# Performance work log

Hardware: AMD Instinct MI355X
Metric: run time of the kernel (lower is better)

The kernel has to match this reference:

```python
import jax, jax.numpy as jnp
import numpy as np

B, S, E, H = 4, 2048, 1024, 16
D = E // H  # head_dim = 64


def setup_inputs() -> dict:
    key = jax.random.key(0)
    k1, k2, k3 = jax.random.split(key, 3)
    x = jax.random.normal(k1, (B, S, E), dtype=jnp.float32)
    w_attn = jax.random.normal(k2, (E, 3 * E), dtype=jnp.float32) * (E ** -0.5)
    b_attn = jnp.zeros((3 * E,), dtype=jnp.float32)
    w_out = jax.random.normal(k3, (E, E), dtype=jnp.float32) * (E ** -0.5)
    b_out = jnp.zeros((E,), dtype=jnp.float32)
    return {"x": x, "w_attn": w_attn, "b_attn": b_attn, "w_out": w_out, "b_out": b_out}


def reference(x, w_attn, b_attn, w_out, b_out):
    b, s, e = x.shape
    qkv = x @ w_attn + b_attn                      # [b, s, 3e]
    q, k, v = jnp.split(qkv, 3, axis=2)
    q = q.reshape(b, s, H, D)
    k = k.reshape(b, s, H, D)
    v = v.reshape(b, s, H, D)
    energy = jnp.einsum('nqhd,nkhd->nhqk', q, k)   # [b, H, s, s]
    causal = jnp.tril(jnp.ones((s, s), dtype=bool))
    energy = jnp.where(causal, energy, -jnp.inf)
    scale = jnp.sqrt(jnp.float32(D))
    attn = jax.nn.softmax(energy / scale, axis=-1)  # dropout_rate=0.0 -> identity
    out = jnp.einsum('nhql,nlhd->nqhd', attn, v).reshape(b, s, e)
    return out @ w_out + b_out
```

## Files before the change

kernel.cpp:

```cpp
#include <hip/hip_runtime.h>

typedef short bf16x8 __attribute__((ext_vector_type(8)));
typedef float f32x4 __attribute__((ext_vector_type(4)));
typedef float f32x16 __attribute__((ext_vector_type(16)));
typedef float float4v __attribute__((ext_vector_type(4)));
typedef short short4v __attribute__((ext_vector_type(4)));
typedef unsigned uint2v __attribute__((ext_vector_type(2)));
typedef unsigned uint4v __attribute__((ext_vector_type(4)));

#define B_ 4
#define S_ 2048
#define E_ 1024
#define H_ 16
#define D_ 64
#define M_ (B_*S_)
#define N1_ (3*E_)

__device__ inline short f2bs(float f) {
    unsigned u = __builtin_bit_cast(unsigned, f);
    unsigned r = u + 0x7fffu + ((u >> 16) & 1u);
    return (short)(r >> 16);
}
__device__ inline float exp2a(float x) {
    float r; asm("v_exp_f32 %0, %1" : "=v"(r) : "v"(x)); return r;
}
__device__ inline unsigned cvtpk(float a, float b) {
    unsigned r; asm("v_cvt_pk_bf16_f32 %0, %1, %2" : "=v"(r) : "v"(a), "v"(b)); return r;
}

__device__ inline const __attribute__((address_space(1))) void* gas(const void* p) {
    return (const __attribute__((address_space(1))) void*)p;
}
__device__ inline __attribute__((address_space(3))) void* las(void* p) {
    return (__attribute__((address_space(3))) void*)p;
}

__global__ void convert_f32_bf16(const float* __restrict__ in, short* __restrict__ out, int n) {
    int tid = blockIdx.x * blockDim.x + threadIdx.x;
    int stride = gridDim.x * blockDim.x;
    for (int i = tid * 4; i < n; i += stride * 4) {
        float4v v = *(const float4v*)&in[i];
        short4v o;
        o[0] = f2bs(v[0]); o[1] = f2bs(v[1]); o[2] = f2bs(v[2]); o[3] = f2bs(v[3]);
        *(short4v*)&out[i] = o;
    }
}

__global__ void transpose_convert(const float* __restrict__ in, short* __restrict__ out,
                                  int rows, int cols) {
    __shared__ float t[32][33];
    int bx = blockIdx.x * 32;
    int by = blockIdx.y * 32;
    int tx = threadIdx.x, ty = threadIdx.y;
#pragma unroll
    for (int i = 0; i < 4; ++i)
        t[ty + i * 8][tx] = in[(size_t)(by + ty + i * 8) * cols + bx + tx];
    __syncthreads();
#pragma unroll
    for (int i = 0; i < 4; ++i)
        out[(size_t)(bx + ty + i * 8) * rows + by + tx] = f2bs(t[tx][ty + i * 8]);
}

#define MFMA12(Q) \
    _Pragma("unroll") for (int mf = 0; mf < 2; ++mf) \
    _Pragma("unroll") for (int nf = 0; nf < 3; ++nf) { \
        acc[(Q)*2+mf][nf] = __builtin_amdgcn_mfma_f32_16x16x32_bf16(af[mf][0], bfrag[nf][0], acc[(Q)*2+mf][nf], 0, 0, 0); \
        acc[(Q)*2+mf][nf] = __builtin_amdgcn_mfma_f32_16x16x32_bf16(af[mf][1], bfrag[nf][1], acc[(Q)*2+mf][nf], 0, 0, 0); \
    }

#define PHASE(Q, STAGE_STMT, WAITV) do { \
    bf16x8 af[2][2]; \
    _Pragma("unroll") for (int mf = 0; mf < 2; ++mf) \
    _Pragma("unroll") for (int ks = 0; ks < 2; ++ks) { \
        int r = (Q)*32 + mf*16 + li; \
        af[mf][ks] = *(const bf16x8*)(lA + r*128 + ((ks*64 + g*16) ^ ((r & 7) << 4))); \
    } \
    STAGE_STMT; \
    __builtin_amdgcn_s_barrier(); \
    asm volatile("s_waitcnt lgkmcnt(0)" ::: "memory"); \
    __builtin_amdgcn_sched_barrier(0); \
    __builtin_amdgcn_s_setprio(1); \
    MFMA12(Q); \
    __builtin_amdgcn_s_setprio(0); \
    WAITV; \
    __builtin_amdgcn_s_barrier(); \
} while (0)

#define VMW(n) asm volatile("s_waitcnt vmcnt(" #n ")" ::: "memory")
#define NOP_ ((void)0)

__global__ __launch_bounds__(512, 2) void gemm_qkv(
    const short* __restrict__ A, const short* __restrict__ Bt,
    const float* __restrict__ bias,
    short* __restrict__ Qb, short* __restrict__ Kb, short* __restrict__ Vt) {
    __shared__ __attribute__((aligned(16))) short ldsA[2][16384];
    __shared__ __attribute__((aligned(16))) short ldsB[2][12288];
    const int tid = threadIdx.x;
    const int lane = tid & 63;
    const int wid = tid >> 6;
    const int li = lane & 15, g = lane >> 4;
    const int wr = wid >> 2, wc = wid & 3;
    const int Kdim = E_;
    const int NT = Kdim >> 6;

    const int id = blockIdx.x;
    const int swz = (id & 7) * 64 + (id >> 3);
    const int bx = swz & 15, by = swz >> 4;
    const int row0 = by * 256, col0 = bx * 192;

    const int rstage = wid * 8 + (lane >> 3);
    const int cstage = (((lane & 7) ^ ((lane >> 3) & 7)) << 4);

    auto stageA = [&](int buf, int kt, int seg) {
#pragma unroll
        for (int h = 0; h < 2; ++h) {
            const char* src = (const char*)A +
                ((size_t)(row0 + h * 128 + seg * 64 + rstage) * Kdim + kt * 64) * 2 + cstage;
            char* dst = (char*)&ldsA[buf][0] + (h * 2 + seg) * 8192 + wid * 1024;
            __builtin_amdgcn_global_load_lds(gas(src), las(dst), 16, 0, 0);
        }
    };
    auto stageB = [&](int buf, int kt) {
#pragma unroll
        for (int i = 0; i < 3; ++i) {
            const char* src = (const char*)Bt +
                ((size_t)(col0 + i * 64 + rstage) * Kdim + kt * 64) * 2 + cstage;
            char* dst = (char*)&ldsB[buf][0] + i * 8192 + wid * 1024;
            __builtin_amdgcn_global_load_lds(gas(src), las(dst), 16, 0, 0);
        }
    };

    f32x4 acc[8][3];
#pragma unroll
    for (int m = 0; m < 8; ++m)
#pragma unroll
        for (int n = 0; n < 3; ++n) acc[m][n] = (f32x4){0.f, 0.f, 0.f, 0.f};

    stageB(0, 0);
    stageA(0, 0, 0);
    stageA(0, 0, 1);
    asm volatile("s_waitcnt vmcnt(0)" ::: "memory");
    __syncthreads();

    for (int t = 0; t < NT; ++t) {
        const int cur = t & 1;
        const int nb = cur ^ 1;
        const int tn = t + 1;
        const bool st = (tn < NT);
        const char* lA = (const char*)&ldsA[cur][0] + wr * 16384;
        const char* lB = (const char*)&ldsB[cur][0];

        bf16x8 bfrag[3][2];
#pragma unroll
        for (int nf = 0; nf < 3; ++nf)
#pragma unroll
            for (int ks = 0; ks < 2; ++ks) {
                int r = wc * 48 + nf * 16 + li;
                bfrag[nf][ks] = *(const bf16x8*)(lB + r * 128 + ((ks * 64 + g * 16) ^ ((r & 7) << 4)));
            }
        if (st) {
            PHASE(0, { stageB(nb, tn); stageA(nb, tn, 0); stageA(nb, tn, 1); }, NOP_);
            PHASE(1, NOP_, VMW(7));
            PHASE(2, NOP_, NOP_);
            PHASE(3, NOP_, VMW(2));
        } else {
            PHASE(0, NOP_, NOP_);
            PHASE(1, NOP_, VMW(0));
            PHASE(2, NOP_, NOP_);
            PHASE(3, NOP_, NOP_);
        }
    }

#pragma unroll
    for (int nf = 0; nf < 3; ++nf) {
        int ncolg = col0 + wc * 48 + nf * 16 + li;
        float bv = bias[ncolg];
        int part = ncolg >> 10;
        int rem = ncolg & 1023;
        if (part < 2) {
            short* Dst = (part == 0) ? Qb : Kb;
#pragma unroll
            for (int mi = 0; mi < 8; ++mi) {
                int rbase = row0 + wr * 128 + mi * 16 + 4 * g;
#pragma unroll
                for (int j = 0; j < 4; ++j)
                    Dst[(size_t)(rbase + j) * E_ + rem] = f2bs(acc[mi][nf][j] + bv);
            }
        } else {
            int h = rem >> 6, d = rem & 63;
#pragma unroll
            for (int mi = 0; mi < 8; ++mi) {
                int s0 = row0 + wr * 128 + mi * 16 + 4 * g;
                int bb2 = s0 >> 11;
                int ss = s0 & 2047;
                uint2v p;
                p[0] = cvtpk(acc[mi][nf][0] + bv, acc[mi][nf][1] + bv);
                p[1] = cvtpk(acc[mi][nf][2] + bv, acc[mi][nf][3] + bv);
                *(uint2v*)&Vt[((size_t)(bb2 * H_ + h) * D_ + d) * S_ + ss] = p;
            }
        }
    }
}

#define MFMA8(Q) \
    _Pragma("unroll") for (int mf = 0; mf < 2; ++mf) \
    _Pragma("unroll") for (int nf = 0; nf < 2; ++nf) { \
        acc[(Q)*2+mf][nf] = __builtin_amdgcn_mfma_f32_16x16x32_bf16(af[mf][0], bfrag[nf][0], acc[(Q)*2+mf][nf], 0, 0, 0); \
        acc[(Q)*2+mf][nf] = __builtin_amdgcn_mfma_f32_16x16x32_bf16(af[mf][1], bfrag[nf][1], acc[(Q)*2+mf][nf], 0, 0, 0); \
    }

#define PHASE8(Q, STAGE_STMT, WAITV) do { \
    bf16x8 af[2][2]; \
    _Pragma("unroll") for (int mf = 0; mf < 2; ++mf) \
    _Pragma("unroll") for (int ks = 0; ks < 2; ++ks) { \
        int r = (Q)*32 + mf*16 + li; \
        af[mf][ks] = *(const bf16x8*)(lA + r*128 + ((ks*64 + g*16) ^ ((r & 7) << 4))); \
    } \
    STAGE_STMT; \
    __builtin_amdgcn_s_barrier(); \
    asm volatile("s_waitcnt lgkmcnt(0)" ::: "memory"); \
    __builtin_amdgcn_sched_barrier(0); \
    __builtin_amdgcn_s_setprio(1); \
    MFMA8(Q); \
    __builtin_amdgcn_s_setprio(0); \
    WAITV; \
    __builtin_amdgcn_s_barrier(); \
} while (0)

__global__ __launch_bounds__(512, 2) void gemm_out8(
    const short* __restrict__ A, const short* __restrict__ Bt,
    const float* __restrict__ bias, float* __restrict__ Cf) {
    __shared__ __attribute__((aligned(16))) short ldsA[2][2][2][4096];
    __shared__ __attribute__((aligned(16))) short ldsB[2][8192];
    const int tid = threadIdx.x;
    const int lane = tid & 63;
    const int wid = tid >> 6;
    const int li = lane & 15, g = lane >> 4;
    const int wr = wid >> 2, wc = wid & 3;
    const int Kdim = E_;
    const int NT = Kdim >> 6;

    const int id = blockIdx.x;
    const int swz = (id & 7) * 32 + (id >> 3);
    const int bx = swz & 7, by = swz >> 3;
    const int row0 = by * 256, col0 = bx * 128;

    const int rstage = wid * 8 + (lane >> 3);
    const int cstage = (((lane & 7) ^ ((lane >> 3) & 7)) << 4);

    auto stageA = [&](int buf, int kt, int seg) {
#pragma unroll
        for (int h = 0; h < 2; ++h) {
            const char* src = (const char*)A +
                ((size_t)(row0 + h * 128 + seg * 64 + rstage) * Kdim + kt * 64) * 2 + cstage;
            char* dst = (char*)&ldsA[buf][h][seg][0] + wid * 1024;
            __builtin_amdgcn_global_load_lds(gas(src), las(dst), 16, 0, 0);
        }
    };
    auto stageB = [&](int buf, int kt) {
#pragma unroll
        for (int i = 0; i < 2; ++i) {
            const char* src = (const char*)Bt +
                ((size_t)(col0 + i * 64 + rstage) * Kdim + kt * 64) * 2 + cstage;
            char* dst = (char*)&ldsB[buf][0] + i * 8192 + wid * 1024;
            __builtin_amdgcn_global_load_lds(gas(src), las(dst), 16, 0, 0);
        }
    };

    f32x4 acc[8][2];
#pragma unroll
    for (int m = 0; m < 8; ++m)
#pragma unroll
        for (int n = 0; n < 2; ++n) acc[m][n] = (f32x4){0.f, 0.f, 0.f, 0.f};

    stageB(0, 0);
    stageA(0, 0, 0);
    stageA(0, 0, 1);
    asm volatile("s_waitcnt vmcnt(0)" ::: "memory");
    __syncthreads();

    for (int t = 0; t < NT; ++t) {
        const int cur = t & 1;
        const int nb = cur ^ 1;
        const int tn = t + 1;
        const bool st = (tn < NT);
        const char* lA = (const char*)&ldsA[cur][wr][0][0];
        const char* lB = (const char*)&ldsB[cur][0];

        bf16x8 bfrag[2][2];
#pragma unroll
        for (int nf = 0; nf < 2; ++nf)
#pragma unroll
            for (int ks = 0; ks < 2; ++ks) {
                int r = wc * 32 + nf * 16 + li;
                bfrag[nf][ks] = *(const bf16x8*)(lB + r * 128 + ((ks * 64 + g * 16) ^ ((r & 7) << 4)));
            }
        if (st) {
            PHASE8(0, stageB(nb, tn), NOP_);
            PHASE8(1, stageA(nb, tn, 0), VMW(4));
            PHASE8(2, stageA(nb, tn, 1), NOP_);
            PHASE8(3, NOP_, VMW(2));
        } else {
            PHASE8(0, NOP_, NOP_);
            PHASE8(1, NOP_, VMW(0));
            PHASE8(2, NOP_, NOP_);
            PHASE8(3, NOP_, NOP_);
        }
    }

#pragma unroll
    for (int nf = 0; nf < 2; ++nf) {
        int ncol = col0 + wc * 32 + nf * 16 + li;
        float bv = bias[ncol];
#pragma unroll
        for (int mi = 0; mi < 8; ++mi) {
            int rbase = row0 + wr * 128 + mi * 16 + 4 * g;
#pragma unroll
            for (int j = 0; j < 4; ++j)
                Cf[(size_t)(rbase + j) * E_ + ncol] = acc[mi][nf][j] + bv;
        }
    }
}

__global__ __launch_bounds__(256, 4) void attn_kernel(
    const short* __restrict__ Qb, const short* __restrict__ Kb,
    const short* __restrict__ Vt, short* __restrict__ Ob) {
    __shared__ __attribute__((aligned(16))) short Kl[4096];
    __shared__ __attribute__((aligned(16))) short Vl[4096];
    const int lane = threadIdx.x & 63;
    const int wv = threadIdx.x >> 6;
    const int l31 = lane & 31;
    const int hi = lane >> 5;
    const int id = blockIdx.x;
    const int xcd = id & 7;
    const int r_ = id >> 3;
    const int qt = 15 - (r_ >> 3);
    const int bh = xcd * 8 + (r_ & 7);
    const int bb = bh >> 4, hh = bh & 15;
    const short* Qh = Qb + (size_t)bb * (S_ * E_) + hh * 64;
    const short* Kh = Kb + (size_t)bb * (S_ * E_) + hh * 64;
    const short* Vh = Vt + (size_t)bh * (D_ * S_);
    const float CEXP = 0.18033688011112042f;

    const int rstage = wv * 8 + (lane >> 3);
    const int cstage = (((lane & 7) ^ ((lane >> 3) & 7)) << 4);

    const int q0w = qt * 128 + wv * 32;
    const int q = q0w + l31;

    bf16x8 qf[4];
#pragma unroll
    for (int c = 0; c < 4; ++c)
        qf[c] = *(const bf16x8*)&Qh[(size_t)q * E_ + c * 16 + hi * 8];

    f32x16 acc[2];
#pragma unroll
    for (int d = 0; d < 2; ++d)
#pragma unroll
        for (int r = 0; r < 16; ++r) acc[d][r] = 0.f;
    float m = -3e38f, mC = 0.f, l = 0.f;

    const int nw = (q0w + 95) >> 6;
    const int nt = (qt * 128 + 191) >> 6;

    for (int it = 0; it < nt; ++it) {
        const int kt0 = it * 64;
#pragma unroll
        for (int half = 0; half < 2; ++half) {
            const char* gk = (const char*)(Kh + (size_t)(kt0 + half * 32 + rstage) * E_) + cstage;
            __builtin_amdgcn_global_load_lds(gas(gk), las((char*)Kl + half * 4096 + wv * 1024), 16, 0, 0);
            const char* gv = (const char*)Vh + (size_t)(half * 32 + rstage) * (S_ * 2) + (size_t)kt0 * 2 + cstage;
            __builtin_amdgcn_global_load_lds(gas(gv), las((char*)Vl + half * 4096 + wv * 1024), 16, 0, 0);
        }
        __syncthreads();
        if (it < nw) {
            f32x16 sc0, sc1;
#pragma unroll
            for (int r = 0; r < 16; ++r) { sc0[r] = 0.f; sc1[r] = 0.f; }
#pragma unroll
            for (int c = 0; c < 4; ++c) {
                const int r0 = l31, r1 = 32 + l31;
                bf16x8 kf0 = *(const bf16x8*)((const char*)Kl + r0 * 128 +
                                              ((c * 32 + hi * 16) ^ ((r0 & 7) << 4)));
                bf16x8 kf1 = *(const bf16x8*)((const char*)Kl + r1 * 128 +
                                              ((c * 32 + hi * 16) ^ ((r1 & 7) << 4)));
                sc0 = __builtin_amdgcn_mfma_f32_32x32x16_bf16(kf0, qf[c], sc0, 0, 0, 0);
                sc1 = __builtin_amdgcn_mfma_f32_32x32x16_bf16(kf1, qf[c], sc1, 0, 0, 0);
            }
            if (kt0 + 63 > q0w) {
                const int kb = kt0 + 4 * hi;
#pragma unroll
                for (int r = 0; r < 16; ++r) {
                    int key = kb + (r & 3) + 8 * (r >> 2);
                    sc0[r] = (key > q) ? -3e38f : sc0[r];
                    sc1[r] = (key + 32 > q) ? -3e38f : sc1[r];
                }
            }
            float tmx[8];
#pragma unroll
            for (int r = 0; r < 8; ++r)
                tmx[r] = fmaxf(fmaxf(sc0[2 * r], sc0[2 * r + 1]),
                               fmaxf(sc1[2 * r], sc1[2 * r + 1]));
            float tm = fmaxf(fmaxf(fmaxf(tmx[0], tmx[1]), fmaxf(tmx[2], tmx[3])),
                             fmaxf(fmaxf(tmx[4], tmx[5]), fmaxf(tmx[6], tmx[7])));
            tm = fmaxf(tm, __shfl_xor(tm, 32, 64));
            bool need = (tm > m + 16.0f);
            if (__ballot((int)need) != 0ull) {
                float mn = fmaxf(m, tm);
                float sf = exp2a((m - mn) * CEXP);
                m = mn; mC = mn * CEXP;
                l *= sf;
#pragma unroll
                for (int d = 0; d < 2; ++d)
#pragma unroll
                    for (int r = 0; r < 16; ++r) acc[d][r] *= sf;
            }
#pragma unroll
            for (int r = 0; r < 16; ++r) {
                sc0[r] = exp2a(fmaf(sc0[r], CEXP, -mC));
                sc1[r] = exp2a(fmaf(sc1[r], CEXP, -mC));
            }
            float s0 = 0.f, s1 = 0.f;
#pragma unroll
            for (int r = 0; r < 8; ++r) {
                s0 += sc0[2 * r] + sc0[2 * r + 1];
                s1 += sc1[2 * r] + sc1[2 * r + 1];
            }
            float ls = s0 + s1;
            ls += __shfl_xor(ls, 32, 64);
            l += ls;
            const bool lo = (hi == 0);
            bf16x8 pf[4];
#pragma unroll
            for (int s = 0; s < 2; ++s) {
                const f32x16& p = s ? sc1 : sc0;
                unsigned W0 = cvtpk(p[0], p[1]),   W1 = cvtpk(p[2], p[3]);
                unsigned W2 = cvtpk(p[4], p[5]),   W3 = cvtpk(p[6], p[7]);
                unsigned W4 = cvtpk(p[8], p[9]),   W5 = cvtpk(p[10], p[11]);
                unsigned W6 = cvtpk(p[12], p[13]), W7 = cvtpk(p[14], p[15]);
                unsigned xW0 = __shfl_xor(W0, 32, 64), xW1 = __shfl_xor(W1, 32, 64);
                unsigned xW2 = __shfl_xor(W2, 32, 64), xW3 = __shfl_xor(W3, 32, 64);
                unsigned xW4 = __shfl_xor(W4, 32, 64), xW5 = __shfl_xor(W5, 32, 64);
                unsigned xW6 = __shfl_xor(W6, 32, 64), xW7 = __shfl_xor(W7, 32, 64);
                uint4v u1, u2;
                u1[0] = lo ? W0 : xW2;  u1[1] = lo ? W1 : xW3;
                u1[2] = lo ? xW0 : W2;  u1[3] = lo ? xW1 : W3;
                u2[0] = lo ? W4 : xW6;  u2[1] = lo ? W5 : xW7;
                u2[2] = lo ? xW4 : W6;  u2[3] = lo ? xW5 : W7;
                pf[s * 2] = __builtin_bit_cast(bf16x8, u1);
                pf[s * 2 + 1] = __builtin_bit_cast(bf16x8, u2);
            }
#pragma unroll
            for (int db = 0; db < 2; ++db) {
                const int row = db * 32 + l31;
                const int rsw = (row & 7) << 4;
                const char* vrow = (const char*)Vl + row * 128;
                bf16x8 v0 = *(const bf16x8*)(vrow + ((hi * 16) ^ rsw));
                bf16x8 v1 = *(const bf16x8*)(vrow + ((32 + hi * 16) ^ rsw));
                bf16x8 v2 = *(const bf16x8*)(vrow + ((64 + hi * 16) ^ rsw));
                bf16x8 v3 = *(const bf16x8*)(vrow + ((96 + hi * 16) ^ rsw));
                acc[db] = __builtin_amdgcn_mfma_f32_32x32x16_bf16(v0, pf[0], acc[db], 0, 0, 0);
                acc[db] = __builtin_amdgcn_mfma_f32_32x32x16_bf16(v1, pf[1], acc[db], 0, 0, 0);
                acc[db] = __builtin_amdgcn_mfma_f32_32x32x16_bf16(v2, pf[2], acc[db], 0, 0, 0);
                acc[db] = __builtin_amdgcn_mfma_f32_32x32x16_bf16(v3, pf[3], acc[db], 0, 0, 0);
            }
        }
        __syncthreads();
    }

    float rl = __builtin_amdgcn_rcpf(l);
    short* orow = Ob + ((size_t)(bb * S_ + q)) * E_ + hh * 64;
#pragma unroll
    for (int db = 0; db < 2; ++db)
#pragma unroll
        for (int rb = 0; rb < 4; ++rb) {
            uint2v pk;
            pk[0] = cvtpk(acc[db][rb * 4 + 0] * rl, acc[db][rb * 4 + 1] * rl);
            pk[1] = cvtpk(acc[db][rb * 4 + 2] * rl, acc[db][rb * 4 + 3] * rl);
            *(uint2v*)&orow[db * 32 + rb * 8 + hi * 4] = pk;
        }
}

extern "C" void kernel_launch(void* const* d_in, const int* in_sizes, int n_in,
                              void* d_out, int out_size, void* d_ws, size_t ws_size,
                              hipStream_t stream) {
    const float* x      = (const float*)d_in[0];
    const float* w_attn = (const float*)d_in[1];
    const float* b_attn = (const float*)d_in[2];
    const float* w_out  = (const float*)d_in[3];
    const float* b_out  = (const float*)d_in[4];
    float* out = (float*)d_out;

    char* ws = (char*)d_ws;
    short* Xbf  = (short*)(ws);
    short* Wat  = (short*)(ws + (16ull << 20));
    short* Wot  = (short*)(ws + (22ull << 20));
    short* Qb   = (short*)(ws + (24ull << 20));
    short* Kb   = (short*)(ws + (40ull << 20));
    short* Vt   = (short*)(ws + (56ull << 20));
    short* Obuf = Xbf;

    convert_f32_bf16<<<2048, 256, 0, stream>>>(x, Xbf, M_ * E_);
    transpose_convert<<<dim3(N1_ / 32, E_ / 32), dim3(32, 8), 0, stream>>>(w_attn, Wat, E_, N1_);
    transpose_convert<<<dim3(E_ / 32, E_ / 32), dim3(32, 8), 0, stream>>>(w_out, Wot, E_, E_);

    gemm_qkv<<<512, 512, 0, stream>>>(Xbf, Wat, b_attn, Qb, Kb, Vt);

    attn_kernel<<<1024, 256, 0, stream>>>(Qb, Kb, Vt, Obuf);

    gemm_out8<<<256, 512, 0, stream>>>(Obuf, Wot, b_out, out);
}
```

Measured before the change: 175.6 us.

## Retile QKV GEMM to 128x192 blocks with 4 waves and 1024 workgroups

```diff
diff --git a/kernel.cpp b/kernel.cpp
--- a/kernel.cpp
+++ b/kernel.cpp
@@ -61,84 +61,82 @@
         out[(size_t)(bx + ty + i * 8) * rows + by + tx] = f2bs(t[tx][ty + i * 8]);
 }
 
-#define MFMA12(Q) \
-    _Pragma("unroll") for (int mf = 0; mf < 2; ++mf) \
-    _Pragma("unroll") for (int nf = 0; nf < 3; ++nf) { \
-        acc[(Q)*2+mf][nf] = __builtin_amdgcn_mfma_f32_16x16x32_bf16(af[mf][0], bfrag[nf][0], acc[(Q)*2+mf][nf], 0, 0, 0); \
-        acc[(Q)*2+mf][nf] = __builtin_amdgcn_mfma_f32_16x16x32_bf16(af[mf][1], bfrag[nf][1], acc[(Q)*2+mf][nf], 0, 0, 0); \
-    }
-
-#define PHASE(Q, STAGE_STMT, WAITV) do { \
-    bf16x8 af[2][2]; \
-    _Pragma("unroll") for (int mf = 0; mf < 2; ++mf) \
-    _Pragma("unroll") for (int ks = 0; ks < 2; ++ks) { \
-        int r = (Q)*32 + mf*16 + li; \
-        af[mf][ks] = *(const bf16x8*)(lA + r*128 + ((ks*64 + g*16) ^ ((r & 7) << 4))); \
-    } \
+#define VMW(n) asm volatile("s_waitcnt vmcnt(" #n ")" ::: "memory")
+#define NOP_ ((void)0)
+
+#define QKV_MFMA(Q) \
+    _Pragma("unroll") for (int nf = 0; nf < 6; ++nf) { \
+        acc[(Q)][nf] = __builtin_amdgcn_mfma_f32_16x16x32_bf16(af[0], bfrag[nf][0], acc[(Q)][nf], 0, 0, 0); \
+        acc[(Q)][nf] = __builtin_amdgcn_mfma_f32_16x16x32_bf16(af[1], bfrag[nf][1], acc[(Q)][nf], 0, 0, 0); \
+    }
+
+#define QKV_PHASE(Q, STAGE_STMT, WAITV) do { \
+    bf16x8 af[2]; \
+    const char* lAq = lA + (Q) * 4096; \
+    _Pragma("unroll") for (int ks = 0; ks < 2; ++ks) \
+        af[ks] = *(const bf16x8*)(lAq + li * 128 + ((ks * 64 + g * 16) ^ ((li & 7) << 4))); \
     STAGE_STMT; \
     __builtin_amdgcn_s_barrier(); \
     asm volatile("s_waitcnt lgkmcnt(0)" ::: "memory"); \
     __builtin_amdgcn_sched_barrier(0); \
     __builtin_amdgcn_s_setprio(1); \
-    MFMA12(Q); \
+    QKV_MFMA(Q); \
     __builtin_amdgcn_s_setprio(0); \
     WAITV; \
     __builtin_amdgcn_s_barrier(); \
 } while (0)
 
-#define VMW(n) asm volatile("s_waitcnt vmcnt(" #n ")" ::: "memory")
-#define NOP_ ((void)0)
-
-__global__ __launch_bounds__(512, 2) void gemm_qkv(
+__global__ __launch_bounds__(256, 2) void gemm_qkv(
     const short* __restrict__ A, const short* __restrict__ Bt,
     const float* __restrict__ bias,
     short* __restrict__ Qb, short* __restrict__ Kb, short* __restrict__ Vt) {
-    __shared__ __attribute__((aligned(16))) short ldsA[2][16384];
+    __shared__ __attribute__((aligned(16))) short ldsA[2][8192];
     __shared__ __attribute__((aligned(16))) short ldsB[2][12288];
     const int tid = threadIdx.x;
     const int lane = tid & 63;
     const int wid = tid >> 6;
     const int li = lane & 15, g = lane >> 4;
-    const int wr = wid >> 2, wc = wid & 3;
+    const int wr = wid >> 1, wc = wid & 1;
     const int Kdim = E_;
     const int NT = Kdim >> 6;
 
     const int id = blockIdx.x;
-    const int swz = (id & 7) * 64 + (id >> 3);
+    const int swz = (id & 7) * 128 + (id >> 3);
     const int bx = swz & 15, by = swz >> 4;
-    const int row0 = by * 256, col0 = bx * 192;
-
-    const int rstage = wid * 8 + (lane >> 3);
-    const int cstage = (((lane & 7) ^ ((lane >> 3) & 7)) << 4);
-
-    auto stageA = [&](int buf, int kt, int seg) {
-#pragma unroll
-        for (int h = 0; h < 2; ++h) {
+    const int row0 = by * 128, col0 = bx * 192;
+
+    const int lr8 = lane >> 3;
+    const int cstage = (((lane & 7) ^ (lr8 & 7)) << 4);
+
+    auto stageA = [&](int buf, int kt) {
+#pragma unroll
+        for (int Q = 0; Q < 4; ++Q) {
+            int grow = (wid >> 1) * 64 + Q * 16 + (wid & 1) * 8 + lr8;
             const char* src = (const char*)A +
-                ((size_t)(row0 + h * 128 + seg * 64 + rstage) * Kdim + kt * 64) * 2 + cstage;
-            char* dst = (char*)&ldsA[buf][0] + (h * 2 + seg) * 8192 + wid * 1024;
+                ((size_t)(row0 + grow) * Kdim + kt * 64) * 2 + cstage;
+            char* dst = (char*)&ldsA[buf][0] + Q * 4096 + wid * 1024;
             __builtin_amdgcn_global_load_lds(gas(src), las(dst), 16, 0, 0);
         }
     };
     auto stageB = [&](int buf, int kt) {
 #pragma unroll
-        for (int i = 0; i < 3; ++i) {
+        for (int i = 0; i < 6; ++i) {
+            int grow = i * 32 + wid * 8 + lr8;
             const char* src = (const char*)Bt +
-                ((size_t)(col0 + i * 64 + rstage) * Kdim + kt * 64) * 2 + cstage;
-            char* dst = (char*)&ldsB[buf][0] + i * 8192 + wid * 1024;
+                ((size_t)(col0 + grow) * Kdim + kt * 64) * 2 + cstage;
+            char* dst = (char*)&ldsB[buf][0] + i * 4096 + wid * 1024;
             __builtin_amdgcn_global_load_lds(gas(src), las(dst), 16, 0, 0);
         }
     };
 
-    f32x4 acc[8][3];
-#pragma unroll
-    for (int m = 0; m < 8; ++m)
-#pragma unroll
-        for (int n = 0; n < 3; ++n) acc[m][n] = (f32x4){0.f, 0.f, 0.f, 0.f};
+    f32x4 acc[4][6];
+#pragma unroll
+    for (int m = 0; m < 4; ++m)
+#pragma unroll
+        for (int n = 0; n < 6; ++n) acc[m][n] = (f32x4){0.f, 0.f, 0.f, 0.f};
 
     stageB(0, 0);
-    stageA(0, 0, 0);
-    stageA(0, 0, 1);
+    stageA(0, 0);
     asm volatile("s_waitcnt vmcnt(0)" ::: "memory");
     __syncthreads();
 
@@ -147,41 +145,41 @@
         const int nb = cur ^ 1;
         const int tn = t + 1;
         const bool st = (tn < NT);
-        const char* lA = (const char*)&ldsA[cur][0] + wr * 16384;
+        const char* lA = (const char*)&ldsA[cur][0] + wr * 2048;
         const char* lB = (const char*)&ldsB[cur][0];
 
-        bf16x8 bfrag[3][2];
-#pragma unroll
-        for (int nf = 0; nf < 3; ++nf)
+        bf16x8 bfrag[6][2];
+#pragma unroll
+        for (int nf = 0; nf < 6; ++nf)
 #pragma unroll
             for (int ks = 0; ks < 2; ++ks) {
-                int r = wc * 48 + nf * 16 + li;
+                int r = wc * 96 + nf * 16 + li;
                 bfrag[nf][ks] = *(const bf16x8*)(lB + r * 128 + ((ks * 64 + g * 16) ^ ((r & 7) << 4)));
             }
         if (st) {
-            PHASE(0, { stageB(nb, tn); stageA(nb, tn, 0); stageA(nb, tn, 1); }, NOP_);
-            PHASE(1, NOP_, VMW(7));
-            PHASE(2, NOP_, NOP_);
-            PHASE(3, NOP_, VMW(2));
+            QKV_PHASE(0, stageB(nb, tn), NOP_);
+            QKV_PHASE(1, stageA(nb, tn), VMW(8));
+            QKV_PHASE(2, NOP_, NOP_);
+            QKV_PHASE(3, NOP_, VMW(2));
         } else {
-            PHASE(0, NOP_, NOP_);
-            PHASE(1, NOP_, VMW(0));
-            PHASE(2, NOP_, NOP_);
-            PHASE(3, NOP_, NOP_);
-        }
-    }
-
-#pragma unroll
-    for (int nf = 0; nf < 3; ++nf) {
-        int ncolg = col0 + wc * 48 + nf * 16 + li;
+            QKV_PHASE(0, NOP_, NOP_);
+            QKV_PHASE(1, NOP_, VMW(0));
+            QKV_PHASE(2, NOP_, NOP_);
+            QKV_PHASE(3, NOP_, NOP_);
+        }
+    }
+
+#pragma unroll
+    for (int nf = 0; nf < 6; ++nf) {
+        int ncolg = col0 + wc * 96 + nf * 16 + li;
         float bv = bias[ncolg];
         int part = ncolg >> 10;
         int rem = ncolg & 1023;
         if (part < 2) {
             short* Dst = (part == 0) ? Qb : Kb;
 #pragma unroll
-            for (int mi = 0; mi < 8; ++mi) {
-                int rbase = row0 + wr * 128 + mi * 16 + 4 * g;
+            for (int mi = 0; mi < 4; ++mi) {
+                int rbase = row0 + wr * 64 + mi * 16 + 4 * g;
 #pragma unroll
                 for (int j = 0; j < 4; ++j)
                     Dst[(size_t)(rbase + j) * E_ + rem] = f2bs(acc[mi][nf][j] + bv);
@@ -189,8 +187,8 @@
         } else {
             int h = rem >> 6, d = rem & 63;
 #pragma unroll
-            for (int mi = 0; mi < 8; ++mi) {
-                int s0 = row0 + wr * 128 + mi * 16 + 4 * g;
+            for (int mi = 0; mi < 4; ++mi) {
+                int s0 = row0 + wr * 64 + mi * 16 + 4 * g;
                 int bb2 = s0 >> 11;
                 int ss = s0 & 2047;
                 uint2v p;
@@ -504,7 +502,7 @@
     transpose_convert<<<dim3(N1_ / 32, E_ / 32), dim3(32, 8), 0, stream>>>(w_attn, Wat, E_, N1_);
     transpose_convert<<<dim3(E_ / 32, E_ / 32), dim3(32, 8), 0, stream>>>(w_out, Wot, E_, E_);
 
-    gemm_qkv<<<512, 512, 0, stream>>>(Xbf, Wat, b_attn, Qb, Kb, Vt);
+    gemm_qkv<<<1024, 256, 0, stream>>>(Xbf, Wat, b_attn, Qb, Kb, Vt);
 
     attn_kernel<<<1024, 256, 0, stream>>>(Qb, Kb, Vt, Obuf);
 
```

Result: faster. 167.6 us (-4.5%).
